# Performance work log

Measured on AMD Instinct MI355X. Metric: run time of the kernel, lower is better.

The kernel has to match this reference:

```python
import jax, jax.numpy as jnp
import numpy as np

B, H, L, D = 8, 8, 2048, 512

def setup_inputs() -> dict:
    key = jax.random.key(0)
    k1, k2 = jax.random.split(key)
    x = jax.random.normal(k1, (B, H, L, D), dtype=jnp.float32)
    mask = jnp.ones((B, L), dtype=jnp.int32)  # unused by the layer's call()
    complex_weight = 0.02 * jax.random.normal(k2, (H, L, D, 2), dtype=jnp.float32)
    return {"x": x, "mask": mask, "complex_weight": complex_weight}

def reference(x, mask, complex_weight):
    # FFT over the innermost (model_size) axis, matching tf.signal.fft
    fft_x = jnp.fft.fft(x.astype(jnp.complex64), axis=-1)
    w = jax.lax.complex(complex_weight[..., 0], complex_weight[..., 1])  # (H, L, D)
    gated = w * fft_x  # broadcast over batch
    out = jnp.fft.ifft(gated, axis=-1).real.astype(jnp.float32)
    return out
```

## Files before the change

### kernel.cpp

```cpp
#include <hip/hip_runtime.h>
#include <math.h>


#define HL    16384
#define NBLK  2048
#define ITERS (HL / NBLK)

__device__ __forceinline__ float2 cadd(float2 a, float2 b){ return make_float2(a.x+b.x, a.y+b.y); }
__device__ __forceinline__ float2 csub(float2 a, float2 b){ return make_float2(a.x-b.x, a.y-b.y); }
__device__ __forceinline__ float2 cmul(float2 a, float2 b){ return make_float2(a.x*b.x - a.y*b.y, a.x*b.y + a.y*b.x); }

__device__ __forceinline__ float2 twiddle(float f) {
    return make_float2(__builtin_amdgcn_cosf(f), -__builtin_amdgcn_sinf(f));
}

__device__ __forceinline__ void twiddle_pows(float f, float2 w[8]) {
    w[1] = twiddle(f);
    w[2] = cmul(w[1], w[1]);
    w[3] = cmul(w[1], w[2]);
    w[4] = cmul(w[2], w[2]);
    w[5] = cmul(w[1], w[4]);
    w[6] = cmul(w[2], w[4]);
    w[7] = cmul(w[3], w[4]);
}

__device__ __forceinline__ void wave_lds_fence() {
    asm volatile("s_waitcnt lgkmcnt(0)" ::: "memory");
    __builtin_amdgcn_wave_barrier();
}

__device__ __forceinline__ void fft8(float2 x[8]) {
    const float c = 0.70710678118654752f;
    float2 u0 = cadd(x[0], x[4]);
    float2 u1 = cadd(x[1], x[5]);
    float2 u2 = cadd(x[2], x[6]);
    float2 u3 = cadd(x[3], x[7]);
    float2 v0 = csub(x[0], x[4]);
    float2 t1 = csub(x[1], x[5]);
    float2 t2 = csub(x[2], x[6]);
    float2 t3 = csub(x[3], x[7]);
    float2 v1 = make_float2(c*(t1.x + t1.y), c*(t1.y - t1.x));
    float2 v2 = make_float2(t2.y, -t2.x);
    float2 v3 = make_float2(c*(t3.y - t3.x), -c*(t3.x + t3.y));
    float2 p0 = cadd(u0, u2), p1 = cadd(u1, u3);
    float2 q0 = csub(u0, u2), q1t = csub(u1, u3);
    float2 q1 = make_float2(q1t.y, -q1t.x);
    x[0] = cadd(p0, p1);
    x[4] = csub(p0, p1);
    x[2] = cadd(q0, q1);
    x[6] = csub(q0, q1);
    float2 r0 = cadd(v0, v2), r1 = cadd(v1, v3);
    float2 s0 = csub(v0, v2), s1t = csub(v1, v3);
    float2 s1 = make_float2(s1t.y, -s1t.x);
    x[1] = cadd(r0, r1);
    x[5] = csub(r0, r1);
    x[3] = cadd(s0, s1);
    x[7] = csub(s0, s1);
}

__device__ __forceinline__ void fft512(float2 v[8], int role, int lane, float2* sc)
{
    fft8(v);
    {
        float2 w[8];
        twiddle_pows((float)role * (1.0f/512.0f), w);
        #pragma unroll
        for (int k = 1; k < 8; ++k) v[k] = cmul(v[k], w[k]);
    }
    wave_lds_fence();
    #pragma unroll
    for (int k1 = 0; k1 < 8; ++k1) sc[k1*72 + role] = v[k1];
    wave_lds_fence();
    const int k1 = lane >> 3, m2 = lane & 7;
    float2 u[8];
    #pragma unroll
    for (int m1 = 0; m1 < 8; ++m1) u[m1] = sc[k1*72 + 8*m1 + m2];
    fft8(u);
    {
        float2 w[8];
        twiddle_pows((float)m2 * (1.0f/64.0f), w);
        #pragma unroll
        for (int j = 1; j < 8; ++j) u[j] = cmul(u[j], w[j]);
    }
    wave_lds_fence();
    #pragma unroll
    for (int j1 = 0; j1 < 8; ++j1) sc[k1*72 + 9*j1 + m2] = u[j1];
    wave_lds_fence();
    const int j1 = lane & 7;
    #pragma unroll
    for (int m = 0; m < 8; ++m) v[m] = sc[k1*72 + 9*j1 + m];
    fft8(v);
}

using gu32 = __attribute__((address_space(1))) const unsigned int;
using lu32 = __attribute__((address_space(3))) unsigned int;

__global__ __launch_bounds__(256) void sgn_fft_pipe(
    const float* __restrict__ x,
    const float* __restrict__ cw,
    float* __restrict__ out)
{
    __shared__ __align__(16) float2 sc[4][8*72];
    __shared__ __align__(16) float  inb[4][2][512];

    const int tid  = threadIdx.x;
    const int wid  = tid >> 6;
    const int lane = tid & 63;
    const int dsl  = ((lane & 7) << 3) | (lane >> 3);

    const float2* __restrict__ cw2 = (const float2*)cw;
    float2* scw = &sc[wid][0];

    {
        const int hl = blockIdx.x;
        const int r1 = (wid       * HL + hl) * 512;
        const int r2 = ((wid + 4) * HL + hl) * 512;
        #pragma unroll
        for (int c = 0; c < 2; ++c) {
            __builtin_amdgcn_global_load_lds((gu32*)(x + r1 + c*256 + lane*4),
                                             (lu32*)(&inb[wid][0][c*256]), 16, 0, 0);
            __builtin_amdgcn_global_load_lds((gu32*)(x + r2 + c*256 + lane*4),
                                             (lu32*)(&inb[wid][1][c*256]), 16, 0, 0);
        }
    }
    asm volatile("s_waitcnt vmcnt(0)" ::: "memory");

    #pragma unroll 1
    for (int it = 0; it < ITERS; ++it) {
        const int hl = blockIdx.x + NBLK * it;
        const int r1 = (wid       * HL + hl) * 512;
        const int r2 = ((wid + 4) * HL + hl) * 512;
        const int wrow = hl * 512;

        asm volatile("s_waitcnt vmcnt(16)" ::: "memory");

        float2 v[8];
        #pragma unroll
        for (int j = 0; j < 8; ++j) {
            v[j].x = inb[wid][0][64*j + lane];
            v[j].y = inb[wid][1][64*j + lane];
        }
        wave_lds_fence();

        if (it + 1 < ITERS) {
            const int hln = hl + NBLK;
            const int r1n = (wid       * HL + hln) * 512;
            const int r2n = ((wid + 4) * HL + hln) * 512;
            #pragma unroll
            for (int c = 0; c < 2; ++c) {
                __builtin_amdgcn_global_load_lds((gu32*)(x + r1n + c*256 + lane*4),
                                                 (lu32*)(&inb[wid][0][c*256]), 16, 0, 0);
                __builtin_amdgcn_global_load_lds((gu32*)(x + r2n + c*256 + lane*4),
                                                 (lu32*)(&inb[wid][1][c*256]), 16, 0, 0);
            }
        }

        float2 wk[8];
        #pragma unroll
        for (int j2 = 0; j2 < 8; ++j2) wk[j2] = cw2[wrow + dsl + 64*j2];

        fft512(v, lane, lane, scw);

        const float hs = 0.5f / 512.0f;
        #pragma unroll
        for (int j2 = 0; j2 < 8; ++j2) {
            const int k  = dsl + 64*j2;
            const int nk = (512 - k) & 511;
            const float2 wnk = cw2[wrow + nk];
            const float2 wp  = make_float2(hs*(wk[j2].x + wnk.x), hs*(wk[j2].y - wnk.y));
            const float2 g   = cmul(wp, v[j2]);
            v[j2] = make_float2(g.x, -g.y);
        }

        fft512(v, dsl, lane, scw);

        #pragma unroll
        for (int j2 = 0; j2 < 8; ++j2) {
            const int k = dsl + 64*j2;
            out[r1 + k] =  v[j2].x;
            out[r2 + k] = -v[j2].y;
        }
    }
}

extern "C" void kernel_launch(void* const* d_in, const int* in_sizes, int n_in,
                              void* d_out, int out_size, void* d_ws, size_t ws_size,
                              hipStream_t stream) {
    const float* x  = (const float*)d_in[0];
    const float* cw = (const float*)d_in[2];
    float* out = (float*)d_out;

    sgn_fft_pipe<<<dim3(NBLK), dim3(256), 0, stream>>>(x, cw, out);
}
```

Baseline: 485.1 us.

## Replace persistent prefetch loop with one-row-per-block kernel and LDS twiddle tables

Drops the persistent 2048-block loop that prefetched input rows into LDS with async global-to-LDS loads. It now launches one block per (head, position) row with 8-block launch bounds, and reads x straight into registers. Twiddle factors are computed once per block into small LDS tables instead of being built from sin/cos and complex multiplies inside each FFT stage. This aims to raise occupancy and cut register pressure and transcendental work, but it gives up explicit load/compute overlap and adds a block-wide barrier plus table setup on every block.

```diff
diff --git a/kernel.cpp b/kernel.cpp
--- a/kernel.cpp
+++ b/kernel.cpp
@@ -2,9 +2,7 @@
 #include <math.h>
 
 
-#define HL    16384
-#define NBLK  2048
-#define ITERS (HL / NBLK)
+#define HL 16384
 
 __device__ __forceinline__ float2 cadd(float2 a, float2 b){ return make_float2(a.x+b.x, a.y+b.y); }
 __device__ __forceinline__ float2 csub(float2 a, float2 b){ return make_float2(a.x-b.x, a.y-b.y); }
@@ -12,16 +10,6 @@
 
 __device__ __forceinline__ float2 twiddle(float f) {
     return make_float2(__builtin_amdgcn_cosf(f), -__builtin_amdgcn_sinf(f));
-}
-
-__device__ __forceinline__ void twiddle_pows(float f, float2 w[8]) {
-    w[1] = twiddle(f);
-    w[2] = cmul(w[1], w[1]);
-    w[3] = cmul(w[1], w[2]);
-    w[4] = cmul(w[2], w[2]);
-    w[5] = cmul(w[1], w[4]);
-    w[6] = cmul(w[2], w[4]);
-    w[7] = cmul(w[3], w[4]);
 }
 
 __device__ __forceinline__ void wave_lds_fence() {
@@ -58,15 +46,13 @@
     x[7] = csub(s0, s1);
 }
 
-__device__ __forceinline__ void fft512(float2 v[8], int role, int lane, float2* sc)
+__device__ __forceinline__ void fft512_t(float2 v[8], int role, int lane, float2* sc,
+                                         const float2* __restrict__ twA,
+                                         const float2* __restrict__ twB)
 {
     fft8(v);
-    {
-        float2 w[8];
-        twiddle_pows((float)role * (1.0f/512.0f), w);
-        #pragma unroll
-        for (int k = 1; k < 8; ++k) v[k] = cmul(v[k], w[k]);
-    }
+    #pragma unroll
+    for (int k = 1; k < 8; ++k) v[k] = cmul(v[k], twA[role*7 + (k-1)]);
     wave_lds_fence();
     #pragma unroll
     for (int k1 = 0; k1 < 8; ++k1) sc[k1*72 + role] = v[k1];
@@ -76,12 +62,8 @@
     #pragma unroll
     for (int m1 = 0; m1 < 8; ++m1) u[m1] = sc[k1*72 + 8*m1 + m2];
     fft8(u);
-    {
-        float2 w[8];
-        twiddle_pows((float)m2 * (1.0f/64.0f), w);
-        #pragma unroll
-        for (int j = 1; j < 8; ++j) u[j] = cmul(u[j], w[j]);
-    }
+    #pragma unroll
+    for (int j = 1; j < 8; ++j) u[j] = cmul(u[j], twB[m2*7 + (j-1)]);
     wave_lds_fence();
     #pragma unroll
     for (int j1 = 0; j1 < 8; ++j1) sc[k1*72 + 9*j1 + m2] = u[j1];
@@ -92,94 +74,67 @@
     fft8(v);
 }
 
-using gu32 = __attribute__((address_space(1))) const unsigned int;
-using lu32 = __attribute__((address_space(3))) unsigned int;
-
-__global__ __launch_bounds__(256) void sgn_fft_pipe(
+__global__ __launch_bounds__(256, 8) void sgn_fft_occ(
     const float* __restrict__ x,
     const float* __restrict__ cw,
     float* __restrict__ out)
 {
     __shared__ __align__(16) float2 sc[4][8*72];
-    __shared__ __align__(16) float  inb[4][2][512];
+    __shared__ __align__(16) float2 twA[64*7];
+    __shared__ __align__(16) float2 twB[8*7];
 
     const int tid  = threadIdx.x;
     const int wid  = tid >> 6;
     const int lane = tid & 63;
     const int dsl  = ((lane & 7) << 3) | (lane >> 3);
+    const int hl   = blockIdx.x;
 
+    {
+        const int role = tid & 63, j = tid >> 6;
+        twA[role*7 + 2*j] = twiddle((float)(role*(2*j+1)) * (1.0f/512.0f));
+        if (j < 3)
+            twA[role*7 + 2*j + 1] = twiddle((float)(role*(2*j+2)) * (1.0f/512.0f));
+        if (tid < 56) {
+            const int m2 = tid / 7, k = tid % 7 + 1;
+            twB[m2*7 + (k-1)] = twiddle((float)(m2*k) * (1.0f/64.0f));
+        }
+    }
+    __syncthreads();
+
+    const int r1 = (wid       * HL + hl) * 512;
+    const int r2 = ((wid + 4) * HL + hl) * 512;
     const float2* __restrict__ cw2 = (const float2*)cw;
+    const int wrow = hl * 512;
     float2* scw = &sc[wid][0];
 
-    {
-        const int hl = blockIdx.x;
-        const int r1 = (wid       * HL + hl) * 512;
-        const int r2 = ((wid + 4) * HL + hl) * 512;
-        #pragma unroll
-        for (int c = 0; c < 2; ++c) {
-            __builtin_amdgcn_global_load_lds((gu32*)(x + r1 + c*256 + lane*4),
-                                             (lu32*)(&inb[wid][0][c*256]), 16, 0, 0);
-            __builtin_amdgcn_global_load_lds((gu32*)(x + r2 + c*256 + lane*4),
-                                             (lu32*)(&inb[wid][1][c*256]), 16, 0, 0);
-        }
+    float2 v[8];
+    #pragma unroll
+    for (int j = 0; j < 8; ++j) {
+        v[j].x = x[r1 + 64*j + lane];
+        v[j].y = x[r2 + 64*j + lane];
     }
-    asm volatile("s_waitcnt vmcnt(0)" ::: "memory");
 
-    #pragma unroll 1
-    for (int it = 0; it < ITERS; ++it) {
-        const int hl = blockIdx.x + NBLK * it;
-        const int r1 = (wid       * HL + hl) * 512;
-        const int r2 = ((wid + 4) * HL + hl) * 512;
-        const int wrow = hl * 512;
+    fft512_t(v, lane, lane, scw, twA, twB);
 
-        asm volatile("s_waitcnt vmcnt(16)" ::: "memory");
+    const float hs = 0.5f / 512.0f;
+    #pragma unroll
+    for (int j2 = 0; j2 < 8; ++j2) {
+        const int k  = dsl + 64*j2;
+        const int nk = (512 - k) & 511;
+        const float2 wk  = cw2[wrow + k];
+        const float2 wnk = cw2[wrow + nk];
+        const float2 wp  = make_float2(hs*(wk.x + wnk.x), hs*(wk.y - wnk.y));
+        const float2 g   = cmul(wp, v[j2]);
+        v[j2] = make_float2(g.x, -g.y);
+    }
 
-        float2 v[8];
-        #pragma unroll
-        for (int j = 0; j < 8; ++j) {
-            v[j].x = inb[wid][0][64*j + lane];
-            v[j].y = inb[wid][1][64*j + lane];
-        }
-        wave_lds_fence();
+    fft512_t(v, dsl, lane, scw, twA, twB);
 
-        if (it + 1 < ITERS) {
-            const int hln = hl + NBLK;
-            const int r1n = (wid       * HL + hln) * 512;
-            const int r2n = ((wid + 4) * HL + hln) * 512;
-            #pragma unroll
-            for (int c = 0; c < 2; ++c) {
-                __builtin_amdgcn_global_load_lds((gu32*)(x + r1n + c*256 + lane*4),
-                                                 (lu32*)(&inb[wid][0][c*256]), 16, 0, 0);
-                __builtin_amdgcn_global_load_lds((gu32*)(x + r2n + c*256 + lane*4),
-                                                 (lu32*)(&inb[wid][1][c*256]), 16, 0, 0);
-            }
-        }
-
-        float2 wk[8];
-        #pragma unroll
-        for (int j2 = 0; j2 < 8; ++j2) wk[j2] = cw2[wrow + dsl + 64*j2];
-
-        fft512(v, lane, lane, scw);
-
-        const float hs = 0.5f / 512.0f;
-        #pragma unroll
-        for (int j2 = 0; j2 < 8; ++j2) {
-            const int k  = dsl + 64*j2;
-            const int nk = (512 - k) & 511;
-            const float2 wnk = cw2[wrow + nk];
-            const float2 wp  = make_float2(hs*(wk[j2].x + wnk.x), hs*(wk[j2].y - wnk.y));
-            const float2 g   = cmul(wp, v[j2]);
-            v[j2] = make_float2(g.x, -g.y);
-        }
-
-        fft512(v, dsl, lane, scw);
-
-        #pragma unroll
-        for (int j2 = 0; j2 < 8; ++j2) {
-            const int k = dsl + 64*j2;
-            out[r1 + k] =  v[j2].x;
-            out[r2 + k] = -v[j2].y;
-        }
+    #pragma unroll
+    for (int j2 = 0; j2 < 8; ++j2) {
+        const int k = dsl + 64*j2;
+        out[r1 + k] =  v[j2].x;
+        out[r2 + k] = -v[j2].y;
     }
 }
 
@@ -190,5 +145,5 @@
     const float* cw = (const float*)d_in[2];
     float* out = (float*)d_out;
 
-    sgn_fft_pipe<<<dim3(NBLK), dim3(256), 0, stream>>>(x, cw, out);
+    sgn_fft_occ<<<dim3(HL), dim3(256), 0, stream>>>(x, cw, out);
 }
```

New measurement: 486.6 us. About the same (+0.3%).
